# Kernel tuning notes

Measured on AMD Instinct MI355X. Metric: run time of the kernel, lower is better.

Reference implementation:

```python
import jax, jax.numpy as jnp
import numpy as np

N = 50000
E = 800000
DIN = 64
DOUT = 64
H = 4
C = DOUT // H
EPS = 1e-5


def setup_inputs() -> dict:
    key = jax.random.key(0)
    ks = jax.random.split(key, 40)
    inp = {}
    inp["x"] = jax.random.normal(ks[0], (N, DIN), jnp.float32)
    inp["edge_index"] = jax.random.randint(ks[1], (2, E), 0, N, dtype=jnp.int32)
    inp["edge_weight"] = jax.random.uniform(ks[2], (E,), jnp.float32)
    inp["edge_attr"] = jax.random.normal(ks[3], (E, 1), jnp.float32)
    k = 4
    for i in range(2):
        din = DIN if i == 0 else DOUT
        s = din ** -0.5
        inp[f"gcn_w{i}"] = jax.random.normal(ks[k], (din, DOUT), jnp.float32) * s; k += 1
        inp[f"gcn_b{i}"] = jnp.zeros((DOUT,), jnp.float32)
        inp[f"res_w{i}"] = jax.random.normal(ks[k], (din, DOUT), jnp.float32) * s; k += 1
        inp[f"res_b{i}"] = jnp.zeros((DOUT,), jnp.float32)
        inp[f"ln_g{i}"] = jnp.ones((DOUT,), jnp.float32)
        inp[f"ln_b{i}"] = jnp.zeros((DOUT,), jnp.float32)
        sg = DOUT ** -0.5
        inp[f"gat_w{i}"] = jax.random.normal(ks[k], (DOUT, H * C), jnp.float32) * sg; k += 1
        inp[f"gat_b{i}"] = jnp.zeros((H * C,), jnp.float32)
        inp[f"att_src{i}"] = jax.random.normal(ks[k], (H, C), jnp.float32) * (C ** -0.5); k += 1
        inp[f"att_dst{i}"] = jax.random.normal(ks[k], (H, C), jnp.float32) * (C ** -0.5); k += 1
        inp[f"att_e{i}"] = jax.random.normal(ks[k], (H, C), jnp.float32) * (C ** -0.5); k += 1
        inp[f"ew_w{i}"] = jax.random.normal(ks[k], (1, H * C), jnp.float32); k += 1
    return inp


def _gcn(x, src0, dst0, ew, W, b):
    n = x.shape[0]
    sl = jnp.arange(n, dtype=src0.dtype)
    src = jnp.concatenate([src0, sl])
    dst = jnp.concatenate([dst0, sl])
    w = jnp.concatenate([ew, jnp.ones((n,), ew.dtype)])  # self-loop weight 1
    deg = jax.ops.segment_sum(w, dst, num_segments=n)
    dinv = jnp.where(deg > 0, jax.lax.rsqrt(deg), 0.0)
    norm = dinv[src] * w * dinv[dst]
    h = x @ W  # [n, DOUT]
    out = jax.ops.segment_sum(h[src] * norm[:, None], dst, num_segments=n)
    return out + b


def _gat(x, src0, dst0, ea, W, b, a_src, a_dst, a_e, We):
    n = x.shape[0]
    sl = jnp.arange(n, dtype=src0.dtype)
    src = jnp.concatenate([src0, sl])
    dst = jnp.concatenate([dst0, sl])
    loop_attr = jnp.broadcast_to(ea.mean(axis=0, keepdims=True), (n, ea.shape[1]))
    ea2 = jnp.concatenate([ea, loop_attr], axis=0)  # fill_value='mean'
    xl = (x @ W).reshape(n, H, C)
    a_s = (xl * a_src).sum(-1)  # [n,H]
    a_d = (xl * a_dst).sum(-1)
    a_ee = ((ea2 @ We).reshape(-1, H, C) * a_e).sum(-1)  # [E2,H]
    alpha = jax.nn.leaky_relu(a_s[src] + a_d[dst] + a_ee, 0.2)
    m = jax.ops.segment_max(alpha, dst, num_segments=n)
    e = jnp.exp(alpha - m[dst])
    s = jax.ops.segment_sum(e, dst, num_segments=n)
    alpha = e / (s[dst] + 1e-16)
    out = jax.ops.segment_sum(xl[src] * alpha[:, :, None], dst, num_segments=n)
    return out.reshape(n, H * C) + b


def _ln(x, g, b):
    mu = x.mean(-1, keepdims=True)
    v = ((x - mu) ** 2).mean(-1, keepdims=True)
    return (x - mu) * jax.lax.rsqrt(v + EPS) * g + b


def reference(x, edge_index, edge_weight, edge_attr,
              gcn_w0, gcn_b0, res_w0, res_b0, ln_g0, ln_b0,
              gat_w0, gat_b0, att_src0, att_dst0, att_e0, ew_w0,
              gcn_w1, gcn_b1, res_w1, res_b1, ln_g1, ln_b1,
              gat_w1, gat_b1, att_src1, att_dst1, att_e1, ew_w1):
    src0, dst0 = edge_index[0], edge_index[1]
    layers = [
        (gcn_w0, gcn_b0, res_w0, res_b0, ln_g0, ln_b0, gat_w0, gat_b0, att_src0, att_dst0, att_e0, ew_w0),
        (gcn_w1, gcn_b1, res_w1, res_b1, ln_g1, ln_b1, gat_w1, gat_b1, att_src1, att_dst1, att_e1, ew_w1),
    ]
    for (gw, gb, rw, rb, lg, lb, Wg, bg, a_s, a_d, a_e, We) in layers:
        residual = x @ rw + rb
        x = jax.nn.silu(_gcn(x, src0, dst0, edge_weight, gw, gb)) + residual
        x = _ln(x, lg, lb)
        x = jax.nn.silu(_gat(x, src0, dst0, edge_attr, Wg, bg, a_s, a_d, a_e, We)) + x
    return x  # down_sample=False -> Identity
```

## Files before the change

kernel.cpp:

```cpp
#include <hip/hip_runtime.h>
#include <hip/hip_fp16.h>

#define NN 50000
#define NE 800000
#define D 64
#define EPS 1e-5f
#define NT 3125
#define NB1 250
#define EPB 3200
#define NBIN 196
#define STOT 49152
#define SBLK 192

typedef unsigned short ushort_t;
typedef unsigned int uint_t;
typedef __attribute__((ext_vector_type(8))) short bf16x8;
typedef __attribute__((ext_vector_type(4))) float f32x4;

__device__ __forceinline__ float wave_sum64(float v) {
#pragma unroll
  for (int m = 1; m <= 32; m <<= 1) v += __shfl_xor(v, m, 64);
  return v;
}
__device__ __forceinline__ float half_sum32(float v) {
#pragma unroll
  for (int m = 1; m <= 16; m <<= 1) v += __shfl_xor(v, m, 64);
  return v;
}
__device__ __forceinline__ int wave_sum64i(int v) {
#pragma unroll
  for (int m = 1; m <= 32; m <<= 1) v += __shfl_xor(v, m, 64);
  return v;
}
__device__ __forceinline__ float group_sum16(float v) {
#pragma unroll
  for (int m = 1; m <= 8; m <<= 1) v += __shfl_xor(v, m, 64);
  return v;
}
__device__ __forceinline__ float silu_f(float v) { return v / (1.f + __expf(-v)); }
__device__ __forceinline__ float lrelu_f(float v) { return v >= 0.f ? v : 0.2f * v; }
__device__ __forceinline__ ushort_t f2b(float x) {
  unsigned u = __float_as_uint(x);
  return (ushort_t)((u + 0x7FFFu + ((u >> 16) & 1u)) >> 16);
}
__device__ __forceinline__ float b2f(ushort_t u) {
  return __uint_as_float(((unsigned)u) << 16);
}
__device__ __forceinline__ float b2f_lo(uint_t u) {
  return __uint_as_float(u << 16);
}
__device__ __forceinline__ float b2f_hi(uint_t u) {
  return __uint_as_float(u & 0xFFFF0000u);
}
__device__ __forceinline__ ushort_t f2h(float x) {
  return __half_as_ushort(__float2half_rn(x));
}
__device__ __forceinline__ float h2f(unsigned u) {
  return __half2float(__ushort_as_half((ushort_t)(u & 0xFFFFu)));
}
__device__ __forceinline__ float sel4(float a, float b, float c, float d, int h) {
  float ab = (h & 1) ? b : a;
  float cd = (h & 1) ? d : c;
  return (h & 2) ? cd : ab;
}
__device__ __forceinline__ bf16x8 pack8(float4 a, float4 b) {
  bf16x8 r;
  r[0] = (short)f2b(a.x); r[1] = (short)f2b(a.y);
  r[2] = (short)f2b(a.z); r[3] = (short)f2b(a.w);
  r[4] = (short)f2b(b.x); r[5] = (short)f2b(b.y);
  r[6] = (short)f2b(b.z); r[7] = (short)f2b(b.w);
  return r;
}

__global__ void __launch_bounds__(256) k_pre(
    const int* __restrict__ ei, int* __restrict__ histG,
    const float* __restrict__ x, const float* __restrict__ W1,
    const float* __restrict__ W2, const float* __restrict__ b2,
    ushort_t* __restrict__ out1, float* __restrict__ out2) {
  __shared__ __align__(16) char smem[16384];
  if (blockIdx.x < NB1) {
    int* h = (int*)smem;
    int blk = blockIdx.x;
    for (int j = threadIdx.x; j < NBIN; j += 256) h[j] = 0;
    __syncthreads();
    int e0 = blk * EPB;
    for (int e = e0 + threadIdx.x; e < e0 + EPB; e += 256)
      atomicAdd(&h[ei[NE + e] >> 8], 1);
    __syncthreads();
    for (int j = threadIdx.x; j < NBIN; j += 256) histG[j * NB1 + blk] = h[j];
    return;
  }
  ushort_t* wf = (ushort_t*)smem;
  for (int e = threadIdx.x; e < 8192; e += 256) {
    int f = e >> 9, r = e & 511;
    int lane = r >> 3, j = r & 7;
    int m = f >> 3, s = (f >> 2) & 1, t = f & 3;
    int k = s * 32 + (lane >> 4) * 8 + j;
    int n = t * 16 + (lane & 15);
    const float* Wm = m ? W2 : W1;
    wf[e] = f2b(Wm[k * D + n]);
  }
  __syncthreads();
  int tile = (blockIdx.x - NB1) * 4 + (threadIdx.x >> 6);
  if (tile >= NT) return;
  int l = threadIdx.x & 63;
  int q = l >> 4, cn = l & 15;
  const float* xr = x + ((size_t)tile * 16 + cn) * D + q * 8;
  float4 xa = *(const float4*)xr;
  float4 xb = *(const float4*)(xr + 4);
  float4 xc = *(const float4*)(xr + 32);
  float4 xd = *(const float4*)(xr + 36);
  bf16x8 a0 = pack8(xa, xb), a1 = pack8(xc, xd);
  f32x4 acc1[4], acc2[4];
#pragma unroll
  for (int t = 0; t < 4; ++t) {
    bf16x8 b10 = *(const bf16x8*)&wf[(0 * 8 + 0 * 4 + t) * 512 + l * 8];
    bf16x8 b11 = *(const bf16x8*)&wf[(0 * 8 + 1 * 4 + t) * 512 + l * 8];
    bf16x8 b20 = *(const bf16x8*)&wf[(1 * 8 + 0 * 4 + t) * 512 + l * 8];
    bf16x8 b21 = *(const bf16x8*)&wf[(1 * 8 + 1 * 4 + t) * 512 + l * 8];
    f32x4 z = {0.f, 0.f, 0.f, 0.f};
    acc1[t] = __builtin_amdgcn_mfma_f32_16x16x32_bf16(a0, b10, z, 0, 0, 0);
    acc1[t] = __builtin_amdgcn_mfma_f32_16x16x32_bf16(a1, b11, acc1[t], 0, 0, 0);
    acc2[t] = __builtin_amdgcn_mfma_f32_16x16x32_bf16(a0, b20, z, 0, 0, 0);
    acc2[t] = __builtin_amdgcn_mfma_f32_16x16x32_bf16(a1, b21, acc2[t], 0, 0, 0);
  }
#pragma unroll
  for (int t = 0; t < 4; ++t) {
    float bb = b2[t * 16 + cn];
#pragma unroll
    for (int r = 0; r < 4; ++r) {
      size_t row = (size_t)tile * 16 + q * 4 + r;
      out1[row * D + t * 16 + cn] = f2b(acc1[t][r]);
      out2[row * D + t * 16 + cn] = acc2[t][r] + bb;
    }
  }
}

__global__ void __launch_bounds__(256) k_scanA(
    int* __restrict__ histG, int* __restrict__ bsum, float* __restrict__ scal,
    const float* __restrict__ Wg0, const float* __restrict__ Wg1,
    const float* __restrict__ W11, const float* __restrict__ W21,
    const float* __restrict__ We0, const float* __restrict__ ae0,
    const float* __restrict__ We1, const float* __restrict__ ae1,
    ushort_t* __restrict__ wg16, ushort_t* __restrict__ wd16,
    float* __restrict__ wea2) {
  if (blockIdx.x == SBLK) {
    int tid = threadIdx.x;
    for (int t = tid; t < 1024; t += 256) scal[t] = 0.f;
    for (int e = tid; e < 4096; e += 256) {
      int f = e >> 9, r = e & 511;
      int lane = r >> 3, j = r & 7;
      int s = (f >> 2) & 1, t = f & 3;
      int k = s * 32 + (lane >> 4) * 8 + j;
      int n = t * 16 + (lane & 15);
      wg16[e] = f2b(Wg0[k * D + n]);
      wg16[4096 + e] = f2b(Wg1[k * D + n]);
    }
    for (int e = tid; e < 8192; e += 256) {
      int f = e >> 9, r = e & 511;
      int lane = r >> 3, j = r & 7;
      int m = f >> 3, s = (f >> 2) & 1, t = f & 3;
      int k = s * 32 + (lane >> 4) * 8 + j;
      int n = t * 16 + (lane & 15);
      const float* Wm = m ? W21 : W11;
      wd16[e] = f2b(Wm[k * D + n]);
    }
    if (tid < 64) {
      float v = group_sum16(We0[tid] * ae0[tid]);
      if ((tid & 15) == 0) wea2[tid >> 4] = v;
    } else if (tid < 128) {
      int c = tid - 64;
      float v = group_sum16(We1[c] * ae1[c]);
      if ((c & 15) == 0) wea2[4 + (c >> 4)] = v;
    }
    return;
  }
  __shared__ int sm[256];
  int j = threadIdx.x;
  int i = blockIdx.x * 256 + j;
  const int TOT = NBIN * NB1;
  int v = (i < TOT) ? histG[i] : 0;
  sm[j] = v;
  __syncthreads();
  for (int off = 1; off < 256; off <<= 1) {
    int t = (j >= off) ? sm[j - off] : 0;
    __syncthreads();
    sm[j] += t;
    __syncthreads();
  }
  if (i < TOT) histG[i] = sm[j] - v;
  if (j == 255) bsum[blockIdx.x] = sm[255];
}

__global__ void __launch_bounds__(256) k_scanC(int* __restrict__ histG,
                                               const int* __restrict__ bsum) {
  __shared__ int ws4[4];
  int t = threadIdx.x;
  int v = (t < (int)blockIdx.x) ? bsum[t] : 0;
  v = wave_sum64i(v);
  if ((t & 63) == 0) ws4[t >> 6] = v;
  __syncthreads();
  int prefix = ws4[0] + ws4[1] + ws4[2] + ws4[3];
  int i = blockIdx.x * 256 + t;
  if (i < NBIN * NB1) histG[i] += prefix;
}

__global__ void __launch_bounds__(256) k_part(
    const int* __restrict__ ei, const float* __restrict__ ew,
    const float* __restrict__ ea, const int* __restrict__ histG,
    uint2* __restrict__ rectmp, float* __restrict__ scal) {
  __shared__ int cur[NBIN];
  int blk = blockIdx.x;
  for (int j = threadIdx.x; j < NBIN; j += 256) cur[j] = histG[j * NB1 + blk];
  __syncthreads();
  int e0 = blk * EPB;
  float asum = 0.f;
  for (int e = e0 + threadIdx.x; e < e0 + EPB; e += 256) {
    int src = ei[e];
    int dst = ei[NE + e];
    float w = ew[e];
    float a = ea[e];
    asum += a;
    int slot = atomicAdd(&cur[dst >> 8], 1);
    uint2 r;
    r.x = (uint_t)(src & 0xFFFF) | ((uint_t)f2h(w) << 16);
    r.y = (uint_t)(dst & 0xFF) | ((uint_t)f2h(a) << 16);
    rectmp[slot] = r;
  }
  float s = wave_sum64(asum);
  if ((threadIdx.x & 63) == 0) {
    int slot = (blk * 4 + (threadIdx.x >> 6)) & 63;
    atomicAdd(&scal[(size_t)slot * 16], s);
  }
}

__global__ void __launch_bounds__(256) k_sfin(
    const uint2* __restrict__ rectmp, const int* __restrict__ histG,
    uint_t* __restrict__ recw, uint_t* __restrict__ reca, int* __restrict__ rs,
    float* __restrict__ dinv, float* __restrict__ scal) {
  __shared__ int cnt[256], sc[256], cur[256];
  __shared__ float wsum[256];
  int b = blockIdx.x;
  int t = threadIdx.x;
  int lo = histG[b * NB1];
  int hi = (b == NBIN - 1) ? NE : histG[(b + 1) * NB1];
  cnt[t] = 0;
  wsum[t] = 0.f;
  __syncthreads();
  for (int e = lo + t; e < hi; e += 256)
    atomicAdd(&cnt[rectmp[e].y & 0xFFu], 1);
  __syncthreads();
  int v = cnt[t];
  sc[t] = v;
  __syncthreads();
  for (int off = 1; off < 256; off <<= 1) {
    int u = (t >= off) ? sc[t - off] : 0;
    __syncthreads();
    sc[t] += u;
    __syncthreads();
  }
  int ex = sc[t] - v;
  int node = b * 256 + t;
  if (node < NN) rs[node] = lo + ex;
  if (b == NBIN - 1 && t == 0) rs[NN] = NE;
  cur[t] = lo + ex;
  __syncthreads();
  for (int e = lo + t; e < hi; e += 256) {
    uint2 r = rectmp[e];
    int dl = (int)(r.y & 0xFFu);
    int slot = atomicAdd(&cur[dl], 1);
    atomicAdd(&wsum[dl], h2f(r.x >> 16));
    uint_t src = r.x & 0xFFFFu;
    recw[slot] = r.x;
    reca[slot] = src | (r.y & 0xFFFF0000u);
  }
  __syncthreads();
  if (node < NN) dinv[node] = rsqrtf(1.f + wsum[t]);
  if (b == 0 && t == 0) {
    float s = 0.f;
    for (int j = 0; j < 64; ++j) s += scal[(size_t)j * 16];
    scal[1] = s / (float)NE;
  }
}

__global__ void __launch_bounds__(256) k_gcn_gat(
    const ushort_t* __restrict__ h16, const float* __restrict__ res,
    const float* __restrict__ dinv, const int* __restrict__ rs,
    const uint_t* __restrict__ recw,
    const float* __restrict__ gb, const float* __restrict__ lg,
    const float* __restrict__ lb,
    const ushort_t* __restrict__ wg, const float* __restrict__ att_src,
    const float* __restrict__ att_dst,
    float* __restrict__ x2, ushort_t* __restrict__ xl,
    float* __restrict__ a_s, float* __restrict__ a_d) {
  __shared__ int ss[4][64];
  __shared__ float swt[4][64];
  __shared__ __align__(16) ushort_t xt[16][72];
  int w = threadIdx.x >> 6;
  int l = threadIdx.x & 63;
  int base = blockIdx.x * 8;
  int half = l >> 5, c = l & 31;
  int iA = base + 2 * w;
  int iB = iA + 1;
  int i = iA + half;
  float di = dinv[i];
  uint_t u0 = *(const uint_t*)&h16[(size_t)i * D + 2 * c];
  float dii = di * di;
  float acc0 = dii * b2f_lo(u0);
  float acc1 = dii * b2f_hi(u0);
  int kA = rs[iA], kA1 = rs[iA + 1];
  int kB = rs[iB], kB1 = rs[iB + 1];
  int sbase = half * 32;
  while (kA < kA1 || kB < kB1) {
    int cntA = min(32, kA1 - kA);
    int cntB = min(32, kB1 - kB);
    int myk = half ? kB : kA;
    int mycnt = half ? cntB : cntA;
    int src = 0; float wn = 0.f;
    if (c < mycnt) {
      uint_t r = recw[(size_t)(myk + c)];
      src = (int)(r & 0xFFFFu);
      wn = dinv[src] * h2f(r >> 16) * di;
    }
    ss[w][l] = src;
    swt[w][l] = wn;
    int nm = max(cntA, cntB);
    int j = 0;
    for (; j + 4 <= nm; j += 4) {
      int4 s4 = *(const int4*)&ss[w][sbase + j];
      float4 w4 = *(const float4*)&swt[w][sbase + j];
      uint_t ua = *(const uint_t*)&h16[(size_t)s4.x * D + 2 * c];
      uint_t ub = *(const uint_t*)&h16[(size_t)s4.y * D + 2 * c];
      uint_t uc = *(const uint_t*)&h16[(size_t)s4.z * D + 2 * c];
      uint_t ud = *(const uint_t*)&h16[(size_t)s4.w * D + 2 * c];
      acc0 = fmaf(w4.x, b2f_lo(ua), acc0); acc1 = fmaf(w4.x, b2f_hi(ua), acc1);
      acc0 = fmaf(w4.y, b2f_lo(ub), acc0); acc1 = fmaf(w4.y, b2f_hi(ub), acc1);
      acc0 = fmaf(w4.z, b2f_lo(uc), acc0); acc1 = fmaf(w4.z, b2f_hi(uc), acc1);
      acc0 = fmaf(w4.w, b2f_lo(ud), acc0); acc1 = fmaf(w4.w, b2f_hi(ud), acc1);
    }
    for (; j < nm; ++j) {
      int s1 = ss[w][sbase + j];
      float w1 = swt[w][sbase + j];
      uint_t u = *(const uint_t*)&h16[(size_t)s1 * D + 2 * c];
      acc0 = fmaf(w1, b2f_lo(u), acc0);
      acc1 = fmaf(w1, b2f_hi(u), acc1);
    }
    kA += cntA; kB += cntB;
  }
  float2 gb2 = *(const float2*)&gb[2 * c];
  float2 lg2 = *(const float2*)&lg[2 * c];
  float2 lb2 = *(const float2*)&lb[2 * c];
  float2 rs2 = *(const float2*)&res[(size_t)i * D + 2 * c];
  float x0 = silu_f(acc0 + gb2.x) + rs2.x;
  float x1 = silu_f(acc1 + gb2.y) + rs2.y;
  float mu = half_sum32(x0 + x1) * (1.f / 64.f);
  float d0 = x0 - mu, d1 = x1 - mu;
  float var = half_sum32(d0 * d0 + d1 * d1) * (1.f / 64.f);
  float rinv = rsqrtf(var + EPS);
  float o0 = d0 * rinv * lg2.x + lb2.x;
  float o1 = d1 * rinv * lg2.y + lb2.y;
  float2 o2; o2.x = o0; o2.y = o1;
  *(float2*)&x2[(size_t)i * D + 2 * c] = o2;
  uint_t pk = (uint_t)f2b(o0) | ((uint_t)f2b(o1) << 16);
  *(uint_t*)&xt[2 * w + half][2 * c] = pk;
  {
    ushort_t* xz = &xt[8][0];
    for (int e = threadIdx.x; e < 8 * 72; e += 256) xz[e] = 0;
  }
  __syncthreads();
  int t = w;
  int q = l >> 4, cn = l & 15;
  bf16x8 a0 = *(const bf16x8*)&xt[cn][q * 8];
  bf16x8 a1 = *(const bf16x8*)&xt[cn][q * 8 + 32];
  bf16x8 b0 = *(const bf16x8*)&wg[(size_t)((0 * 4 + t) * 512 + l * 8)];
  bf16x8 b1 = *(const bf16x8*)&wg[(size_t)((1 * 4 + t) * 512 + l * 8)];
  f32x4 z = {0.f, 0.f, 0.f, 0.f};
  f32x4 acc = __builtin_amdgcn_mfma_f32_16x16x32_bf16(a0, b0, z, 0, 0, 0);
  acc = __builtin_amdgcn_mfma_f32_16x16x32_bf16(a1, b1, acc, 0, 0, 0);
  if (q < 2) {
    float av = att_src[t * 16 + cn];
    float dv = att_dst[t * 16 + cn];
#pragma unroll
    for (int r = 0; r < 4; ++r) {
      size_t row = (size_t)base + q * 4 + r;
      xl[row * D + t * 16 + cn] = f2b(acc[r]);
      float vs = group_sum16(acc[r] * av);
      float vd = group_sum16(acc[r] * dv);
      if (cn == 0) {
        a_s[row * 4 + t] = vs;
        a_d[row * 4 + t] = vd;
      }
    }
  }
}

template <int FUSE>
__global__ void __launch_bounds__(256) k_gat_fin(
    const ushort_t* __restrict__ xl16, const float* __restrict__ x2,
    const float* __restrict__ a_s, const float* __restrict__ a_d,
    const int* __restrict__ rs, const uint_t* __restrict__ reca,
    const float* __restrict__ wea, const float* __restrict__ scal,
    const float* __restrict__ bg,
    const ushort_t* __restrict__ wd, const float* __restrict__ b2,
    ushort_t* __restrict__ out1, float* __restrict__ out2,
    float* __restrict__ xout) {
  __shared__ int ss[4][64];
  __shared__ float el[4][4][68];
  __shared__ __align__(16) ushort_t xt[16][72];
  int w = threadIdx.x >> 6;
  int l = threadIdx.x & 63;
  int base = blockIdx.x * 8;
  int half = l >> 5, c = l & 31;
  int iA = base + 2 * w;
  int iB = iA + 1;
  int i = iA + half;
  int hh = c >> 3;
  float4 wv4 = *(const float4*)wea;
  float mean_attr = scal[1];
  float we_h = sel4(wv4.x, wv4.y, wv4.z, wv4.w, hh);
  float ad_h = a_d[(size_t)i * 4 + hh];
  float as_i = a_s[(size_t)i * 4 + hh];
  float eS = __expf(lrelu_f(as_i + ad_h + mean_attr * we_h));
  float s = eS;
  uint_t u0 = *(const uint_t*)&xl16[(size_t)i * D + 2 * c];
  float acc0 = eS * b2f_lo(u0);
  float acc1 = eS * b2f_hi(u0);
  float4 ad4 = *(const float4*)(a_d + (size_t)i * 4);
  int kA = rs[iA], kA1 = rs[iA + 1];
  int kB = rs[iB], kB1 = rs[iB + 1];
  int sbase = half * 32;
  while (kA < kA1 || kB < kB1) {
    int cntA = min(32, kA1 - kA);
    int cntB = min(32, kB1 - kB);
    int myk = half ? kB : kA;
    int mycnt = half ? cntB : cntA;
    int src = 0;
    float e0v = 0.f, e1v = 0.f, e2v = 0.f, e3v = 0.f;
    if (c < mycnt) {
      uint_t r = reca[(size_t)(myk + c)];
      src = (int)(r & 0xFFFFu);
      float ea = h2f(r >> 16);
      float4 as4 = *(const float4*)(a_s + (size_t)src * 4);
      e0v = __expf(lrelu_f(as4.x + fmaf(ea, wv4.x, ad4.x)));
      e1v = __expf(lrelu_f(as4.y + fmaf(ea, wv4.y, ad4.y)));
      e2v = __expf(lrelu_f(as4.z + fmaf(ea, wv4.z, ad4.z)));
      e3v = __expf(lrelu_f(as4.w + fmaf(ea, wv4.w, ad4.w)));
    }
    ss[w][l] = src;
    el[w][0][l] = e0v;
    el[w][1][l] = e1v;
    el[w][2][l] = e2v;
    el[w][3][l] = e3v;
    int nm = max(cntA, cntB);
    int j = 0;
    for (; j + 4 <= nm; j += 4) {
      int4 s4 = *(const int4*)&ss[w][sbase + j];
      float4 e4 = *(const float4*)&el[w][hh][sbase + j];
      uint_t ua = *(const uint_t*)&xl16[(size_t)s4.x * D + 2 * c];
      uint_t ub = *(const uint_t*)&xl16[(size_t)s4.y * D + 2 * c];
      uint_t uc = *(const uint_t*)&xl16[(size_t)s4.z * D + 2 * c];
      uint_t ud = *(const uint_t*)&xl16[(size_t)s4.w * D + 2 * c];
      acc0 = fmaf(e4.x, b2f_lo(ua), acc0); acc1 = fmaf(e4.x, b2f_hi(ua), acc1);
      acc0 = fmaf(e4.y, b2f_lo(ub), acc0); acc1 = fmaf(e4.y, b2f_hi(ub), acc1);
      acc0 = fmaf(e4.z, b2f_lo(uc), acc0); acc1 = fmaf(e4.z, b2f_hi(uc), acc1);
      acc0 = fmaf(e4.w, b2f_lo(ud), acc0); acc1 = fmaf(e4.w, b2f_hi(ud), acc1);
      s += (e4.x + e4.y) + (e4.z + e4.w);
    }
    for (; j < nm; ++j) {
      int s1 = ss[w][sbase + j];
      float e1 = el[w][hh][sbase + j];
      uint_t u = *(const uint_t*)&xl16[(size_t)s1 * D + 2 * c];
      acc0 = fmaf(e1, b2f_lo(u), acc0);
      acc1 = fmaf(e1, b2f_hi(u), acc1);
      s += e1;
    }
    kA += cntA; kB += cntB;
  }
  float2 bg2 = *(const float2*)&bg[2 * c];
  float rcp = 1.f / (s + 1e-16f);
  float o0 = acc0 * rcp + bg2.x;
  float o1 = acc1 * rcp + bg2.y;
  float2 x22 = *(const float2*)&x2[(size_t)i * D + 2 * c];
  float v0 = silu_f(o0) + x22.x;
  float v1 = silu_f(o1) + x22.y;
  if (FUSE) {
    uint_t pk = (uint_t)f2b(v0) | ((uint_t)f2b(v1) << 16);
    *(uint_t*)&xt[2 * w + half][2 * c] = pk;
    {
      ushort_t* xz = &xt[8][0];
      for (int e = threadIdx.x; e < 8 * 72; e += 256) xz[e] = 0;
    }
    __syncthreads();
    int t = w;
    int q = l >> 4, cn = l & 15;
    bf16x8 a0 = *(const bf16x8*)&xt[cn][q * 8];
    bf16x8 a1 = *(const bf16x8*)&xt[cn][q * 8 + 32];
#pragma unroll
    for (int m = 0; m < 2; ++m) {
      bf16x8 b0 = *(const bf16x8*)&wd[(size_t)((m * 8 + 0 * 4 + t) * 512 + l * 8)];
      bf16x8 b1 = *(const bf16x8*)&wd[(size_t)((m * 8 + 1 * 4 + t) * 512 + l * 8)];
      f32x4 z = {0.f, 0.f, 0.f, 0.f};
      f32x4 acc = __builtin_amdgcn_mfma_f32_16x16x32_bf16(a0, b0, z, 0, 0, 0);
      acc = __builtin_amdgcn_mfma_f32_16x16x32_bf16(a1, b1, acc, 0, 0, 0);
      if (q < 2) {
        float bb = (m == 1) ? b2[t * 16 + cn] : 0.f;
#pragma unroll
        for (int r = 0; r < 4; ++r) {
          size_t row = (size_t)base + q * 4 + r;
          if (m == 0)
            out1[row * D + t * 16 + cn] = f2b(acc[r]);
          else
            out2[row * D + t * 16 + cn] = acc[r] + bb;
        }
      }
    }
  } else {
    float2 v2; v2.x = v0; v2.y = v1;
    *(float2*)&xout[(size_t)i * D + 2 * c] = v2;
  }
}


extern "C" void kernel_launch(void* const* d_in, const int* in_sizes, int n_in,
                              void* d_out, int out_size, void* d_ws, size_t ws_size,
                              hipStream_t stream) {
  (void)in_sizes; (void)n_in; (void)out_size; (void)ws_size;
  const float* x  = (const float*)d_in[0];
  const int*   ei = (const int*)d_in[1];
  const float* ew = (const float*)d_in[2];
  const float* ea = (const float*)d_in[3];
  const float* P[2][12];
  for (int l = 0; l < 2; ++l)
    for (int j = 0; j < 12; ++j) P[l][j] = (const float*)d_in[4 + l * 12 + j];

  float* W = (float*)d_ws;
  const size_t o_rs    = 0;
  const size_t o_dinv  = o_rs + NN + 16;
  const size_t o_wea   = o_dinv + NN;
  const size_t o_scal  = o_wea + 16;
  const size_t o_bsum  = o_scal + 1024;
  const size_t o_hist  = o_bsum + 256;
  const size_t o_recw  = o_hist + STOT;
  const size_t o_reca  = o_recw + NE;
  const size_t o_rtmp  = o_reca + NE;
  const size_t o_h16   = o_rtmp + (size_t)NE * 2;
  const size_t o_xl16  = o_h16 + (size_t)NN * D / 2;
  const size_t o_res   = o_xl16 + (size_t)NN * D / 2;
  const size_t o_x2    = o_res + (size_t)NN * D;
  const size_t o_as    = o_x2 + (size_t)NN * D;
  const size_t o_ad    = o_as + (size_t)NN * 4;
  const size_t o_wg16  = o_ad + (size_t)NN * 4;
  const size_t o_wd16  = o_wg16 + 4096;

  int*      rs    = (int*)(W + o_rs);
  float*    dinv  = W + o_dinv;
  float*    wea2  = W + o_wea;
  float*    scal  = W + o_scal;
  int*      bsum  = (int*)(W + o_bsum);
  int*      histG = (int*)(W + o_hist);
  uint_t*   recw  = (uint_t*)(W + o_recw);
  uint_t*   reca  = (uint_t*)(W + o_reca);
  uint2*    rtmp  = (uint2*)(W + o_rtmp);
  ushort_t* h16   = (ushort_t*)(W + o_h16);
  ushort_t* xl16  = (ushort_t*)(W + o_xl16);
  float*    resb  = W + o_res;
  float*    x2b   = W + o_x2;
  float*    asb   = W + o_as;
  float*    adb   = W + o_ad;
  ushort_t* wg16  = (ushort_t*)(W + o_wg16);
  ushort_t* wd16  = (ushort_t*)(W + o_wd16);

  const int B = 256;
  const int gPre = NB1 + (NT + 3) / 4;
  const int gN2  = NN / 8;

  k_pre<<<gPre, B, 0, stream>>>(ei, histG, x, P[0][0], P[0][2], P[0][3], h16, resb);
  k_scanA<<<SBLK + 1, B, 0, stream>>>(histG, bsum, scal,
                                      P[0][6], P[1][6], P[1][0], P[1][2],
                                      P[0][11], P[0][10], P[1][11], P[1][10],
                                      wg16, wd16, wea2);
  k_scanC<<<SBLK, B, 0, stream>>>(histG, bsum);
  k_part<<<NB1, B, 0, stream>>>(ei, ew, ea, histG, rtmp, scal);
  k_sfin<<<NBIN, B, 0, stream>>>(rtmp, histG, recw, reca, rs, dinv, scal);

  k_gcn_gat<<<gN2, B, 0, stream>>>(h16, resb, dinv, rs, recw,
                                   P[0][1], P[0][4], P[0][5],
                                   wg16, P[0][8], P[0][9],
                                   x2b, xl16, asb, adb);
  k_gat_fin<1><<<gN2, B, 0, stream>>>(xl16, x2b, asb, adb, rs, reca,
                                      wea2, scal, P[0][7],
                                      wd16, P[1][3], h16, resb, nullptr);
  k_gcn_gat<<<gN2, B, 0, stream>>>(h16, resb, dinv, rs, recw,
                                   P[1][1], P[1][4], P[1][5],
                                   wg16 + 4096, P[1][8], P[1][9],
                                   x2b, xl16, asb, adb);
  k_gat_fin<0><<<gN2, B, 0, stream>>>(xl16, x2b, asb, adb, rs, reca,
                                      wea2 + 4, scal, P[1][7],
                                      nullptr, nullptr, nullptr, nullptr,
                                      (float*)d_out);
}
```

Baseline: 285.5 us.

## Fold scan fixup into consumers, move x GEMM into sort-finish, stage bins in LDS

Removes the k_scanC launch. k_part and the sort-finish kernel now each redo the 192-entry block-sum prefix scan locally. The layer-0 x@W GEMM moves out of the histogram kernel and runs as extra blocks of the sort-finish kernel, so it overlaps with the bucket sort instead of the histogram pass. Each bin's records are staged in LDS (up to CAP entries, with a global-memory fallback for overflow), so rectmp is read from global memory once instead of twice. The cost is roughly 51KB of LDS per block, which limits occupancy, plus a redundant scan in every block.

```diff
diff --git a/kernel.cpp b/kernel.cpp
--- a/kernel.cpp
+++ b/kernel.cpp
@@ -11,6 +11,7 @@
 #define NBIN 196
 #define STOT 49152
 #define SBLK 192
+#define CAP 5888
 
 typedef unsigned short ushort_t;
 typedef unsigned int uint_t;
@@ -25,11 +26,6 @@
 __device__ __forceinline__ float half_sum32(float v) {
 #pragma unroll
   for (int m = 1; m <= 16; m <<= 1) v += __shfl_xor(v, m, 64);
-  return v;
-}
-__device__ __forceinline__ int wave_sum64i(int v) {
-#pragma unroll
-  for (int m = 1; m <= 32; m <<= 1) v += __shfl_xor(v, m, 64);
   return v;
 }
 __device__ __forceinline__ float group_sum16(float v) {
@@ -72,68 +68,17 @@
   return r;
 }
 
-__global__ void __launch_bounds__(256) k_pre(
-    const int* __restrict__ ei, int* __restrict__ histG,
-    const float* __restrict__ x, const float* __restrict__ W1,
-    const float* __restrict__ W2, const float* __restrict__ b2,
-    ushort_t* __restrict__ out1, float* __restrict__ out2) {
-  __shared__ __align__(16) char smem[16384];
-  if (blockIdx.x < NB1) {
-    int* h = (int*)smem;
-    int blk = blockIdx.x;
-    for (int j = threadIdx.x; j < NBIN; j += 256) h[j] = 0;
-    __syncthreads();
-    int e0 = blk * EPB;
-    for (int e = e0 + threadIdx.x; e < e0 + EPB; e += 256)
-      atomicAdd(&h[ei[NE + e] >> 8], 1);
-    __syncthreads();
-    for (int j = threadIdx.x; j < NBIN; j += 256) histG[j * NB1 + blk] = h[j];
-    return;
-  }
-  ushort_t* wf = (ushort_t*)smem;
-  for (int e = threadIdx.x; e < 8192; e += 256) {
-    int f = e >> 9, r = e & 511;
-    int lane = r >> 3, j = r & 7;
-    int m = f >> 3, s = (f >> 2) & 1, t = f & 3;
-    int k = s * 32 + (lane >> 4) * 8 + j;
-    int n = t * 16 + (lane & 15);
-    const float* Wm = m ? W2 : W1;
-    wf[e] = f2b(Wm[k * D + n]);
-  }
-  __syncthreads();
-  int tile = (blockIdx.x - NB1) * 4 + (threadIdx.x >> 6);
-  if (tile >= NT) return;
-  int l = threadIdx.x & 63;
-  int q = l >> 4, cn = l & 15;
-  const float* xr = x + ((size_t)tile * 16 + cn) * D + q * 8;
-  float4 xa = *(const float4*)xr;
-  float4 xb = *(const float4*)(xr + 4);
-  float4 xc = *(const float4*)(xr + 32);
-  float4 xd = *(const float4*)(xr + 36);
-  bf16x8 a0 = pack8(xa, xb), a1 = pack8(xc, xd);
-  f32x4 acc1[4], acc2[4];
-#pragma unroll
-  for (int t = 0; t < 4; ++t) {
-    bf16x8 b10 = *(const bf16x8*)&wf[(0 * 8 + 0 * 4 + t) * 512 + l * 8];
-    bf16x8 b11 = *(const bf16x8*)&wf[(0 * 8 + 1 * 4 + t) * 512 + l * 8];
-    bf16x8 b20 = *(const bf16x8*)&wf[(1 * 8 + 0 * 4 + t) * 512 + l * 8];
-    bf16x8 b21 = *(const bf16x8*)&wf[(1 * 8 + 1 * 4 + t) * 512 + l * 8];
-    f32x4 z = {0.f, 0.f, 0.f, 0.f};
-    acc1[t] = __builtin_amdgcn_mfma_f32_16x16x32_bf16(a0, b10, z, 0, 0, 0);
-    acc1[t] = __builtin_amdgcn_mfma_f32_16x16x32_bf16(a1, b11, acc1[t], 0, 0, 0);
-    acc2[t] = __builtin_amdgcn_mfma_f32_16x16x32_bf16(a0, b20, z, 0, 0, 0);
-    acc2[t] = __builtin_amdgcn_mfma_f32_16x16x32_bf16(a1, b21, acc2[t], 0, 0, 0);
-  }
-#pragma unroll
-  for (int t = 0; t < 4; ++t) {
-    float bb = b2[t * 16 + cn];
-#pragma unroll
-    for (int r = 0; r < 4; ++r) {
-      size_t row = (size_t)tile * 16 + q * 4 + r;
-      out1[row * D + t * 16 + cn] = f2b(acc1[t][r]);
-      out2[row * D + t * 16 + cn] = acc2[t][r] + bb;
-    }
-  }
+__global__ void __launch_bounds__(256) k_hist(const int* __restrict__ ei,
+                                              int* __restrict__ histG) {
+  __shared__ int h[NBIN];
+  int blk = blockIdx.x;
+  for (int j = threadIdx.x; j < NBIN; j += 256) h[j] = 0;
+  __syncthreads();
+  int e0 = blk * EPB;
+  for (int e = e0 + threadIdx.x; e < e0 + EPB; e += 256)
+    atomicAdd(&h[ei[NE + e] >> 8], 1);
+  __syncthreads();
+  for (int j = threadIdx.x; j < NBIN; j += 256) histG[j * NB1 + blk] = h[j];
 }
 
 __global__ void __launch_bounds__(256) k_scanA(
@@ -192,30 +137,36 @@
   if (j == 255) bsum[blockIdx.x] = sm[255];
 }
 
-__global__ void __launch_bounds__(256) k_scanC(int* __restrict__ histG,
-                                               const int* __restrict__ bsum) {
-  __shared__ int ws4[4];
-  int t = threadIdx.x;
-  int v = (t < (int)blockIdx.x) ? bsum[t] : 0;
-  v = wave_sum64i(v);
-  if ((t & 63) == 0) ws4[t >> 6] = v;
-  __syncthreads();
-  int prefix = ws4[0] + ws4[1] + ws4[2] + ws4[3];
-  int i = blockIdx.x * 256 + t;
-  if (i < NBIN * NB1) histG[i] += prefix;
-}
-
 __global__ void __launch_bounds__(256) k_part(
     const int* __restrict__ ei, const float* __restrict__ ew,
     const float* __restrict__ ea, const int* __restrict__ histG,
+    const int* __restrict__ bsum,
     uint2* __restrict__ rectmp, float* __restrict__ scal) {
   __shared__ int cur[NBIN];
+  __shared__ int pex[256];
   int blk = blockIdx.x;
-  for (int j = threadIdx.x; j < NBIN; j += 256) cur[j] = histG[j * NB1 + blk];
+  int t = threadIdx.x;
+  int v0 = (t < SBLK) ? bsum[t] : 0;
+  pex[t] = v0;
+  __syncthreads();
+  for (int off = 1; off < 256; off <<= 1) {
+    int u = (t >= off) ? pex[t - off] : 0;
+    __syncthreads();
+    pex[t] += u;
+    __syncthreads();
+  }
+  int ex0 = pex[t] - v0;
+  __syncthreads();
+  pex[t] = ex0;
+  __syncthreads();
+  for (int j = t; j < NBIN; j += 256) {
+    int idx = j * NB1 + blk;
+    cur[j] = histG[idx] + pex[idx >> 8];
+  }
   __syncthreads();
   int e0 = blk * EPB;
   float asum = 0.f;
-  for (int e = e0 + threadIdx.x; e < e0 + EPB; e += 256) {
+  for (int e = e0 + t; e < e0 + EPB; e += 256) {
     int src = ei[e];
     int dst = ei[NE + e];
     float w = ew[e];
@@ -228,26 +179,107 @@
     rectmp[slot] = r;
   }
   float s = wave_sum64(asum);
-  if ((threadIdx.x & 63) == 0) {
-    int slot = (blk * 4 + (threadIdx.x >> 6)) & 63;
+  if ((t & 63) == 0) {
+    int slot = (blk * 4 + (t >> 6)) & 63;
     atomicAdd(&scal[(size_t)slot * 16], s);
   }
 }
 
-__global__ void __launch_bounds__(256) k_sfin(
+__global__ void __launch_bounds__(256) k_sfing(
     const uint2* __restrict__ rectmp, const int* __restrict__ histG,
+    const int* __restrict__ bsum,
     uint_t* __restrict__ recw, uint_t* __restrict__ reca, int* __restrict__ rs,
-    float* __restrict__ dinv, float* __restrict__ scal) {
-  __shared__ int cnt[256], sc[256], cur[256];
-  __shared__ float wsum[256];
+    float* __restrict__ dinv, float* __restrict__ scal,
+    const float* __restrict__ x, const float* __restrict__ W1,
+    const float* __restrict__ W2, const float* __restrict__ b2,
+    ushort_t* __restrict__ out1, float* __restrict__ out2) {
+  __shared__ __align__(16) char smem[4096 + CAP * 8];
+  int t = threadIdx.x;
+  if (blockIdx.x >= NBIN) {
+    ushort_t* wf = (ushort_t*)smem;
+    for (int e = t; e < 8192; e += 256) {
+      int f = e >> 9, r = e & 511;
+      int lane = r >> 3, j = r & 7;
+      int m = f >> 3, s = (f >> 2) & 1, tt = f & 3;
+      int k = s * 32 + (lane >> 4) * 8 + j;
+      int n = tt * 16 + (lane & 15);
+      const float* Wm = m ? W2 : W1;
+      wf[e] = f2b(Wm[k * D + n]);
+    }
+    __syncthreads();
+    int tile = (blockIdx.x - NBIN) * 4 + (t >> 6);
+    if (tile >= NT) return;
+    int l = t & 63;
+    int q = l >> 4, cn = l & 15;
+    const float* xr = x + ((size_t)tile * 16 + cn) * D + q * 8;
+    float4 xa = *(const float4*)xr;
+    float4 xb = *(const float4*)(xr + 4);
+    float4 xc = *(const float4*)(xr + 32);
+    float4 xd = *(const float4*)(xr + 36);
+    bf16x8 a0 = pack8(xa, xb), a1 = pack8(xc, xd);
+    f32x4 acc1[4], acc2[4];
+#pragma unroll
+    for (int tt = 0; tt < 4; ++tt) {
+      bf16x8 b10 = *(const bf16x8*)&wf[(0 * 8 + 0 * 4 + tt) * 512 + l * 8];
+      bf16x8 b11 = *(const bf16x8*)&wf[(0 * 8 + 1 * 4 + tt) * 512 + l * 8];
+      bf16x8 b20 = *(const bf16x8*)&wf[(1 * 8 + 0 * 4 + tt) * 512 + l * 8];
+      bf16x8 b21 = *(const bf16x8*)&wf[(1 * 8 + 1 * 4 + tt) * 512 + l * 8];
+      f32x4 z = {0.f, 0.f, 0.f, 0.f};
+      acc1[tt] = __builtin_amdgcn_mfma_f32_16x16x32_bf16(a0, b10, z, 0, 0, 0);
+      acc1[tt] = __builtin_amdgcn_mfma_f32_16x16x32_bf16(a1, b11, acc1[tt], 0, 0, 0);
+      acc2[tt] = __builtin_amdgcn_mfma_f32_16x16x32_bf16(a0, b20, z, 0, 0, 0);
+      acc2[tt] = __builtin_amdgcn_mfma_f32_16x16x32_bf16(a1, b21, acc2[tt], 0, 0, 0);
+    }
+#pragma unroll
+    for (int tt = 0; tt < 4; ++tt) {
+      float bb = b2[tt * 16 + cn];
+#pragma unroll
+      for (int r = 0; r < 4; ++r) {
+        size_t row = (size_t)tile * 16 + q * 4 + r;
+        out1[row * D + tt * 16 + cn] = f2b(acc1[tt][r]);
+        out2[row * D + tt * 16 + cn] = acc2[tt][r] + bb;
+      }
+    }
+    return;
+  }
+  int* cnt = (int*)smem;
+  int* sc  = cnt + 256;
+  int* cur = sc + 256;
+  float* wsum = (float*)(cur + 256);
+  uint2* lrec = (uint2*)(smem + 4096);
   int b = blockIdx.x;
-  int t = threadIdx.x;
-  int lo = histG[b * NB1];
-  int hi = (b == NBIN - 1) ? NE : histG[(b + 1) * NB1];
+  int v0 = (t < SBLK) ? bsum[t] : 0;
+  sc[t] = v0;
+  __syncthreads();
+  for (int off = 1; off < 256; off <<= 1) {
+    int u = (t >= off) ? sc[t - off] : 0;
+    __syncthreads();
+    sc[t] += u;
+    __syncthreads();
+  }
+  int ex0 = sc[t] - v0;
+  __syncthreads();
+  sc[t] = ex0;
+  __syncthreads();
+  int i0 = b * NB1;
+  int lo = histG[i0] + sc[i0 >> 8];
+  int hi;
+  if (b == NBIN - 1) {
+    hi = NE;
+  } else {
+    int i1 = (b + 1) * NB1;
+    hi = histG[i1] + sc[i1 >> 8];
+  }
+  __syncthreads();
   cnt[t] = 0;
   wsum[t] = 0.f;
   __syncthreads();
-  for (int e = lo + t; e < hi; e += 256)
+  int nc = min(hi - lo, CAP);
+  for (int e = t; e < nc; e += 256) lrec[e] = rectmp[lo + e];
+  __syncthreads();
+  for (int e = t; e < nc; e += 256)
+    atomicAdd(&cnt[lrec[e].y & 0xFFu], 1);
+  for (int e = lo + CAP + t; e < hi; e += 256)
     atomicAdd(&cnt[rectmp[e].y & 0xFFu], 1);
   __syncthreads();
   int v = cnt[t];
@@ -265,7 +297,16 @@
   if (b == NBIN - 1 && t == 0) rs[NN] = NE;
   cur[t] = lo + ex;
   __syncthreads();
-  for (int e = lo + t; e < hi; e += 256) {
+  for (int e = t; e < nc; e += 256) {
+    uint2 r = lrec[e];
+    int dl = (int)(r.y & 0xFFu);
+    int slot = atomicAdd(&cur[dl], 1);
+    atomicAdd(&wsum[dl], h2f(r.x >> 16));
+    uint_t src = r.x & 0xFFFFu;
+    recw[slot] = r.x;
+    reca[slot] = src | (r.y & 0xFFFF0000u);
+  }
+  for (int e = lo + CAP + t; e < hi; e += 256) {
     uint2 r = rectmp[e];
     int dl = (int)(r.y & 0xFFu);
     int slot = atomicAdd(&cur[dl], 1);
@@ -571,17 +612,17 @@
   ushort_t* wd16  = (ushort_t*)(W + o_wd16);
 
   const int B = 256;
-  const int gPre = NB1 + (NT + 3) / 4;
-  const int gN2  = NN / 8;
-
-  k_pre<<<gPre, B, 0, stream>>>(ei, histG, x, P[0][0], P[0][2], P[0][3], h16, resb);
+  const int gSf = NBIN + (NT + 3) / 4;
+  const int gN2 = NN / 8;
+
+  k_hist<<<NB1, B, 0, stream>>>(ei, histG);
   k_scanA<<<SBLK + 1, B, 0, stream>>>(histG, bsum, scal,
                                       P[0][6], P[1][6], P[1][0], P[1][2],
                                       P[0][11], P[0][10], P[1][11], P[1][10],
                                       wg16, wd16, wea2);
-  k_scanC<<<SBLK, B, 0, stream>>>(histG, bsum);
-  k_part<<<NB1, B, 0, stream>>>(ei, ew, ea, histG, rtmp, scal);
-  k_sfin<<<NBIN, B, 0, stream>>>(rtmp, histG, recw, reca, rs, dinv, scal);
+  k_part<<<NB1, B, 0, stream>>>(ei, ew, ea, histG, bsum, rtmp, scal);
+  k_sfing<<<gSf, B, 0, stream>>>(rtmp, histG, bsum, recw, reca, rs, dinv, scal,
+                                 x, P[0][0], P[0][2], P[0][3], h16, resb);
 
   k_gcn_gat<<<gN2, B, 0, stream>>>(h16, resb, dinv, rs, recw,
                                    P[0][1], P[0][4], P[0][5],
```

Result: faster. 277.2 us (-2.9%).
